# Optimization experiments

Measured on AMD Instinct MI355X. Metric: run time of the kernel, lower is better.

Reference implementation:

```python
import jax, jax.numpy as jnp
import numpy as np

B, S, D, H = 4, 1024, 1024, 16
HD = D // H  # head_dim = 64


def setup_inputs() -> dict:
    key = jax.random.key(0)
    ks = jax.random.split(key, 16)
    w = lambda k: jax.random.normal(k, (D, D), dtype=jnp.float32) * 0.02
    b = lambda k: jax.random.normal(k, (D,), dtype=jnp.float32) * 0.02
    x = jax.random.normal(ks[0], (B, S, D), dtype=jnp.float32)
    mask = jnp.tril(jnp.ones((S, S), dtype=jnp.int32))[None, None]  # causal [1,1,S,S]
    bar_indices = jax.random.randint(ks[1], (S,), 0, S, dtype=jnp.int64)
    beat_indices = jax.random.randint(ks[2], (S,), 0, S, dtype=jnp.int64)
    return {
        "x": x, "mask": mask, "bar_indices": bar_indices, "beat_indices": beat_indices,
        "Wq": w(ks[3]), "bq": b(ks[4]), "Wk": w(ks[5]), "bk": b(ks[6]),
        "Wv": w(ks[7]), "bv": b(ks[8]),
        "W_bark": w(ks[9]), "b_bark": b(ks[10]),
        "W_beatk": w(ks[11]), "b_beatk": b(ks[12]),
        "Wo": w(ks[13]), "bo": b(ks[14]),
    }


def reference(x, mask, bar_indices, beat_indices, Wq, bq, Wk, bk, Wv, bv,
              W_bark, b_bark, W_beatk, b_beatk, Wo, bo):
    Bs, Sl, Dm = x.shape
    heads, hd = H, Dm // H

    def proj(t, W, b):  # torch Linear: t @ W.T + b, then split heads -> [B,H,S,hd]
        y = t @ W.T + b
        return y.reshape(Bs, -1, heads, hd).transpose(0, 2, 1, 3)

    q = proj(x, Wq, bq)
    k = proj(x, Wk, bk)
    v = proj(x, Wv, bv)
    scale = 1.0 / jnp.sqrt(jnp.asarray(hd, x.dtype))

    scores = jnp.einsum('bhqd,bhkd->bhqk', q, k) * scale

    # hierarchical bar bias (bar_query is computed but unused in the original)
    bar_k = proj(x[:, bar_indices], W_bark, b_bark)
    scores = scores + 0.2 * (jnp.einsum('bhqd,bhkd->bhqk', q, bar_k) * scale)

    # hierarchical beat bias
    beat_k = proj(x[:, beat_indices], W_beatk, b_beatk)
    scores = scores + 0.1 * (jnp.einsum('bhqd,bhkd->bhqk', q, beat_k) * scale)

    scores = jnp.where(mask == 0, jnp.asarray(-1e9, scores.dtype), scores)
    attn = jax.nn.softmax(scores, axis=-1)  # dropout is identity in eval

    out = jnp.einsum('bhqk,bhkd->bhqd', attn, v)
    out = out.transpose(0, 2, 1, 3).reshape(Bs, Sl, Dm)
    return out @ Wo.T + bo
```

## Files before the change

kernel.cpp:

```cpp
#include <hip/hip_runtime.h>
#include <hip/hip_bf16.h>


typedef __bf16 bf16x8 __attribute__((ext_vector_type(8)));
typedef __bf16 bf16x4 __attribute__((ext_vector_type(4)));
typedef float  f32x4  __attribute__((ext_vector_type(4)));

#define DMODEL 1024

#define ASYNC_LOAD16(gp, lp)                                                  \
    __builtin_amdgcn_global_load_lds(                                         \
        (const __attribute__((address_space(1))) unsigned int*)(gp),          \
        (__attribute__((address_space(3))) unsigned int*)(lp), 16, 0, 0)

__global__ __launch_bounds__(256) void cvt_kernel(
    const float* __restrict__ x,
    const float* __restrict__ Wq, const float* __restrict__ Wk,
    const float* __restrict__ Wv, const float* __restrict__ Wbar,
    const float* __restrict__ Wbeat, const float* __restrict__ Wo,
    __bf16* __restrict__ dst)
{
    const int g = blockIdx.x * 256 + threadIdx.x;
    const size_t e = (size_t)g * 8;
    const int seg = (int)(e >> 20);
    const float* src; size_t off; float s = 1.0f;
    if (seg < 4)       { src = x;     off = e; }
    else if (seg == 4) { src = Wq;    off = e - ((size_t)4 << 20); }
    else if (seg == 5) { src = Wk;    off = e - ((size_t)5 << 20); }
    else if (seg == 6) { src = Wv;    off = e - ((size_t)6 << 20); }
    else if (seg == 7) { src = Wbar;  off = e - ((size_t)7 << 20); s = 0.2f; }
    else if (seg == 8) { src = Wbeat; off = e - ((size_t)8 << 20); s = 0.1f; }
    else               { src = Wo;    off = e - ((size_t)9 << 20); }
    const float4 a = *(const float4*)&src[off];
    const float4 b = *(const float4*)&src[off + 4];
    bf16x8 v;
    v[0] = (__bf16)(a.x * s); v[1] = (__bf16)(a.y * s);
    v[2] = (__bf16)(a.z * s); v[3] = (__bf16)(a.w * s);
    v[4] = (__bf16)(b.x * s); v[5] = (__bf16)(b.y * s);
    v[6] = (__bf16)(b.z * s); v[7] = (__bf16)(b.w * s);
    *(bf16x8*)&dst[e] = v;
}


#define SWZ_COL(r_, ks_) \
    (((((ks_) * 64) + quad * 16) ^ (((r_) & 7) << 4)) >> 1)

#define READ_A(c_, mh_)                                                       \
    do {                                                                      \
        _Pragma("unroll") for (int mi = 0; mi < 2; ++mi) {                    \
            const int r_ = ((w >> 2) << 5) + (mh_) * 64 + mi * 16 + l15;      \
            _Pragma("unroll") for (int ks = 0; ks < 2; ++ks)                  \
                af[mi][ks] = *(const bf16x8*)&Alds[(c_) * 8192 + r_ * 64 +    \
                                                   SWZ_COL(r_, ks)];          \
        }                                                                     \
    } while (0)

#define READ_B(c_, nh_)                                                       \
    do {                                                                      \
        _Pragma("unroll") for (int nj = 0; nj < 2; ++nj) {                    \
            const int r_ = ((w & 3) << 5) + (nh_) * 128 + nj * 16 + l15;      \
            _Pragma("unroll") for (int ks = 0; ks < 2; ++ks)                  \
                bf[nj][ks] = *(const bf16x8*)&Blds[(c_) * 16384 + r_ * 64 +   \
                                                    SWZ_COL(r_, ks)];         \
        }                                                                     \
    } while (0)

#define STAGE_A8(bufn_, h_, kt_)                                              \
    do {                                                                      \
        const int tm_ = (kt_) >> 4;                                           \
        const int k0_ = ((kt_) & 15) << 6;                                    \
        const __bf16* ap_ = (tm_ == 0) ? aA0##h_ : (tm_ == 1) ? aA1##h_       \
                                                              : aA2##h_;      \
        ASYNC_LOAD16(ap_ + k0_,                                               \
                     &Alds[(bufn_) * 8192 + (h_) * 4096 + w * 512]);          \
    } while (0)

#define STAGE_B8(bufn_, h_, kt_)                                              \
    do {                                                                      \
        const int tm_ = (kt_) >> 4;                                           \
        const int k0_ = ((kt_) & 15) << 6;                                    \
        const __bf16* wp_ = (tm_ == 0) ? W0 : (tm_ == 1) ? W1 : W2;           \
        ASYNC_LOAD16(wp_ + bro##h_##0 + k0_,                                  \
                     &Blds[(bufn_) * 16384 + (h_) * 8192 + w * 512]);         \
        ASYNC_LOAD16(wp_ + bro##h_##1 + k0_,                                  \
                     &Blds[(bufn_) * 16384 + (h_) * 8192 + 4096 + w * 512]);  \
    } while (0)

#define PHASE_BAR1()                                                          \
    do {                                                                      \
        __builtin_amdgcn_s_barrier();                                         \
        asm volatile("s_waitcnt lgkmcnt(0)" ::: "memory");                    \
    } while (0)

#define MFMA8(mh_, nh_)                                                       \
    do {                                                                      \
        __builtin_amdgcn_s_setprio(1);                                        \
        _Pragma("unroll") for (int mi = 0; mi < 2; ++mi)                      \
        _Pragma("unroll") for (int nj = 0; nj < 2; ++nj) {                    \
            acc[(mh_)*2 + mi][(nh_)*2 + nj] =                                 \
                __builtin_amdgcn_mfma_f32_16x16x32_bf16(                      \
                    af[mi][0], bf[nj][0], acc[(mh_)*2 + mi][(nh_)*2 + nj],    \
                    0, 0, 0);                                                 \
            acc[(mh_)*2 + mi][(nh_)*2 + nj] =                                 \
                __builtin_amdgcn_mfma_f32_16x16x32_bf16(                      \
                    af[mi][1], bf[nj][1], acc[(mh_)*2 + mi][(nh_)*2 + nj],    \
                    0, 0, 0);                                                 \
        }                                                                     \
        __builtin_amdgcn_s_setprio(0);                                        \
    } while (0)

__global__ __launch_bounds__(512, 2) void gemm8p_kernel(
    const __bf16* __restrict__ xb,
    const __bf16* __restrict__ Wqb, const __bf16* __restrict__ Wkb,
    const __bf16* __restrict__ Wvb, const __bf16* __restrict__ Wbarb,
    const __bf16* __restrict__ Wbeatb,
    const float* __restrict__ bq, const float* __restrict__ bk,
    const float* __restrict__ bv, const float* __restrict__ bbar,
    const float* __restrict__ bbeat,
    const int* __restrict__ bar_idx, const int* __restrict__ beat_idx,
    __bf16* __restrict__ qbuf, __bf16* __restrict__ keffbuf,
    __bf16* __restrict__ vtbuf)
{
    __shared__ __align__(16) __bf16 Alds[2 * 8192];
    __shared__ __align__(16) __bf16 Blds[2 * 16384];

    const int bid = blockIdx.x;
    int mode, tk;
    if (bid < 128)      { mode = 1; tk = bid; }
    else if (bid < 256) { mode = 0; tk = bid - 128; }
    else                { mode = 2; tk = bid - 256; }
    const int m0 = (tk >> 2) << 7;
    const int n0 = (tk & 3) << 8;
    const int nkt = (mode == 1) ? 48 : 16;

    const int t    = (int)threadIdx.x;
    const int w    = t >> 6;
    const int lane = t & 63;
    const int l15  = lane & 15;
    const int quad = lane >> 4;

    const int srow = t >> 3;
    const int scol = ((((t & 7) * 16) ^ (((t >> 3) & 7) << 4)) >> 1);

    const __bf16* aA00 = xb + (size_t)(m0 + srow) * DMODEL + scol;
    const __bf16* aA01 = xb + (size_t)(m0 + 64 + srow) * DMODEL + scol;
    const __bf16* aA10 = aA00; const __bf16* aA11 = aA01;
    const __bf16* aA20 = aA00; const __bf16* aA21 = aA01;
    const __bf16 *W0, *W1, *W2;
    if (mode == 0)      { W0 = W1 = W2 = Wqb; }
    else if (mode == 2) { W0 = W1 = W2 = Wvb; }
    else {
        W0 = Wkb; W1 = Wbarb; W2 = Wbeatb;
        const int bb = m0 & ~1023;
        const int lr = m0 & 1023;
        aA10 = xb + (size_t)(bb + bar_idx[lr + srow]) * DMODEL + scol;
        aA11 = xb + (size_t)(bb + bar_idx[lr + 64 + srow]) * DMODEL + scol;
        aA20 = xb + (size_t)(bb + beat_idx[lr + srow]) * DMODEL + scol;
        aA21 = xb + (size_t)(bb + beat_idx[lr + 64 + srow]) * DMODEL + scol;
    }
    const size_t bro00 = (size_t)(n0 + srow) * DMODEL + scol;
    const size_t bro01 = (size_t)(n0 + 64 + srow) * DMODEL + scol;
    const size_t bro10 = (size_t)(n0 + 128 + srow) * DMODEL + scol;
    const size_t bro11 = (size_t)(n0 + 192 + srow) * DMODEL + scol;

    f32x4 acc[4][4];
#pragma unroll
    for (int i = 0; i < 4; ++i)
#pragma unroll
        for (int j = 0; j < 4; ++j)
            acc[i][j] = {0.f, 0.f, 0.f, 0.f};
    bf16x8 af[2][2], bf[2][2];

    STAGE_A8(0, 0, 0);
    asm volatile("" ::: "memory");
    STAGE_B8(0, 0, 0);
    asm volatile("" ::: "memory");
    STAGE_B8(0, 1, 0);
    asm volatile("" ::: "memory");
    STAGE_A8(0, 1, 0);
    asm volatile("s_waitcnt vmcnt(3)" ::: "memory");
    __builtin_amdgcn_s_barrier();

#pragma unroll 1
    for (int kt = 0; kt < nkt - 1; ++kt) {
        const int c  = kt & 1;
        const int nb = c ^ 1;
        const int kn = kt + 1;

        READ_A(c, 0);
        READ_B(c, 0);
        STAGE_A8(nb, 0, kn);
        PHASE_BAR1();
        MFMA8(0, 0);
        asm volatile("s_waitcnt vmcnt(2)" ::: "memory");
        __builtin_amdgcn_s_barrier();

        READ_B(c, 1);
        STAGE_B8(nb, 0, kn);
        PHASE_BAR1();
        MFMA8(0, 1);
        asm volatile("s_waitcnt vmcnt(3)" ::: "memory");
        __builtin_amdgcn_s_barrier();

        READ_A(c, 1);
        STAGE_B8(nb, 1, kn);
        PHASE_BAR1();
        MFMA8(1, 1);
        __builtin_amdgcn_s_barrier();

        READ_B(c, 0);
        STAGE_A8(nb, 1, kn);
        PHASE_BAR1();
        MFMA8(1, 0);
        asm volatile("s_waitcnt vmcnt(3)" ::: "memory");
        __builtin_amdgcn_s_barrier();
    }

    {
        const int c = (nkt - 1) & 1;
        READ_A(c, 0);
        READ_B(c, 0);
        PHASE_BAR1();
        MFMA8(0, 0);
        asm volatile("s_waitcnt vmcnt(1)" ::: "memory");
        __builtin_amdgcn_s_barrier();

        READ_B(c, 1);
        PHASE_BAR1();
        MFMA8(0, 1);
        asm volatile("s_waitcnt vmcnt(0)" ::: "memory");
        __builtin_amdgcn_s_barrier();

        READ_A(c, 1);
        PHASE_BAR1();
        MFMA8(1, 1);
        __builtin_amdgcn_s_barrier();

        READ_B(c, 0);
        PHASE_BAR1();
        MFMA8(1, 0);
    }

#pragma unroll
    for (int an = 0; an < 4; ++an) {
        const int col = n0 + ((w & 3) << 5) + (an >> 1) * 128 +
                        (an & 1) * 16 + l15;
        float bias;
        if (mode == 0)      bias = bq[col];
        else if (mode == 1) bias = bk[col] + 0.2f * bbar[col] + 0.1f * bbeat[col];
        else                bias = bv[col];
#pragma unroll
        for (int am = 0; am < 4; ++am) {
            const int rowbase = m0 + ((w >> 2) << 5) + (am >> 1) * 64 +
                                (am & 1) * 16 + quad * 4;
            if (mode == 2) {
                const int bb = rowbase >> 10;
                const int sb = rowbase & 1023;
                bf16x4 vv;
#pragma unroll
                for (int r = 0; r < 4; ++r) vv[r] = (__bf16)(acc[am][an][r] + bias);
                *(bf16x4*)&vtbuf[((size_t)(bb * 1024 + col)) * 1024 + sb] = vv;
            } else if (mode == 0) {
#pragma unroll
                for (int r = 0; r < 4; ++r)
                    qbuf[(size_t)(rowbase + r) * DMODEL + col] =
                        (__bf16)((acc[am][an][r] + bias) * 0.125f);
            } else {
#pragma unroll
                for (int r = 0; r < 4; ++r)
                    keffbuf[(size_t)(rowbase + r) * DMODEL + col] =
                        (__bf16)(acc[am][an][r] + bias);
            }
        }
    }
}

__global__ __launch_bounds__(256) void oproj_kernel(
    const __bf16* __restrict__ attnb, const __bf16* __restrict__ Wob,
    const float* __restrict__ bo, float* __restrict__ outb)
{
    const int tile = blockIdx.x;
    const int m0 = (tile >> 3) << 6;
    const int n0 = (tile & 7) << 7;

    __shared__ __align__(16) __bf16 Alds[64 * 32];
    __shared__ __align__(16) __bf16 Blds[128 * 32];

    const int t    = threadIdx.x;
    const int w    = t >> 6;
    const int lane = t & 63;
    const int l15  = lane & 15;
    const int quad = lane >> 4;
    const int wm   = (w >> 1) << 5;
    const int wn   = (w & 1) << 6;
    const int srow = t >> 2;
    const int scol = ((((t & 3) * 16) ^ (((t >> 2) & 3) << 4)) >> 1);
    const int rcol = (((quad * 16) ^ ((l15 & 3) << 4)) >> 1);

    const __bf16* gA  = attnb + (size_t)(m0 + srow) * DMODEL + scol;
    const __bf16* gB0 = Wob + (size_t)(n0 + srow) * DMODEL + scol;
    const __bf16* gB1 = Wob + (size_t)(n0 + 64 + srow) * DMODEL + scol;
    __bf16* lA  = &Alds[w * 512];
    __bf16* lB0 = &Blds[w * 512];
    __bf16* lB1 = &Blds[2048 + w * 512];

    f32x4 acc[2][4];
    for (int i = 0; i < 2; ++i)
        for (int j = 0; j < 4; ++j)
            acc[i][j] = {0.f, 0.f, 0.f, 0.f};

    for (int kk = 0; kk < 32; ++kk) {
        const int k0 = kk * 32;
        ASYNC_LOAD16(gA + k0, lA);
        ASYNC_LOAD16(gB0 + k0, lB0);
        ASYNC_LOAD16(gB1 + k0, lB1);
        __syncthreads();

        bf16x8 af[2], bfr[4];
        for (int i = 0; i < 2; ++i)
            af[i] = *(const bf16x8*)&Alds[(wm + i * 16 + l15) * 32 + rcol];
        for (int j = 0; j < 4; ++j)
            bfr[j] = *(const bf16x8*)&Blds[(wn + j * 16 + l15) * 32 + rcol];

        for (int i = 0; i < 2; ++i)
            for (int j = 0; j < 4; ++j)
                acc[i][j] = __builtin_amdgcn_mfma_f32_16x16x32_bf16(
                    af[i], bfr[j], acc[i][j], 0, 0, 0);
        __syncthreads();
    }

    for (int j = 0; j < 4; ++j) {
        const int col = n0 + wn + j * 16 + l15;
        const float bias = bo[col];
        for (int i = 0; i < 2; ++i) {
            const int rowbase = m0 + wm + i * 16 + quad * 4;
            for (int r = 0; r < 4; ++r)
                outb[(size_t)(rowbase + r) * DMODEL + col] = acc[i][j][r] + bias;
        }
    }
}

__global__ __launch_bounds__(256) void attn_kernel(
    const __bf16* __restrict__ qbuf, const __bf16* __restrict__ keffbuf,
    const __bf16* __restrict__ vtbuf, __bf16* __restrict__ attnbuf)
{
    const int bh = blockIdx.y;
    const int b  = bh >> 4;
    const int h  = bh & 15;
    const int qt = blockIdx.x;
    const int q0 = qt * 64;

    __shared__ __align__(16) __bf16 Klds[64][72];
    __shared__ __align__(16) __bf16 Vlds[64][72];
    __shared__ __align__(16) __bf16 Plds[4][16][72];

    const int t    = threadIdx.x;
    const int w    = t >> 6;
    const int lane = t & 63;
    const int l15  = lane & 15;
    const int quad = lane >> 4;

    const __bf16* qbase =
        qbuf + (size_t)(b * 1024 + q0 + w * 16 + l15) * DMODEL + h * 64;
    bf16x8 qf0 = *(const bf16x8*)&qbase[quad * 8];
    bf16x8 qf1 = *(const bf16x8*)&qbase[32 + quad * 8];

    bf16x8 ones;
    for (int i = 0; i < 8; ++i) ones[i] = (__bf16)1.0f;

    f32x4 o[4];
    for (int i = 0; i < 4; ++i) o[i] = {0.f, 0.f, 0.f, 0.f};
    f32x4 lacc = {0.f, 0.f, 0.f, 0.f};

    const int srow = t >> 2;
    const int scol = (t & 3) * 16;

    const __bf16* kbase = keffbuf + (size_t)(b * 1024) * DMODEL + h * 64;
    const __bf16* vtb   = vtbuf + (size_t)(b * 1024 + h * 64) * 1024;

    for (int j = 0; j <= qt; ++j) {
        const __bf16* kg = kbase + (size_t)(j * 64 + srow) * DMODEL + scol;
        *(bf16x8*)&Klds[srow][scol]     = *(const bf16x8*)kg;
        *(bf16x8*)&Klds[srow][scol + 8] = *(const bf16x8*)(kg + 8);
        const __bf16* vg = vtb + (size_t)srow * 1024 + j * 64 + scol;
        *(bf16x8*)&Vlds[srow][scol]     = *(const bf16x8*)vg;
        *(bf16x8*)&Vlds[srow][scol + 8] = *(const bf16x8*)(vg + 8);
        __syncthreads();

        f32x4 sc[4];
        for (int nt = 0; nt < 4; ++nt) {
            sc[nt] = {0.f, 0.f, 0.f, 0.f};
            bf16x8 kf0 = *(const bf16x8*)&Klds[nt * 16 + l15][quad * 8];
            bf16x8 kf1 = *(const bf16x8*)&Klds[nt * 16 + l15][32 + quad * 8];
            sc[nt] = __builtin_amdgcn_mfma_f32_16x16x32_bf16(qf0, kf0, sc[nt], 0, 0, 0);
            sc[nt] = __builtin_amdgcn_mfma_f32_16x16x32_bf16(qf1, kf1, sc[nt], 0, 0, 0);
        }

        if (j == qt) {
            const int qrow_base = q0 + w * 16 + quad * 4;
            for (int nt = 0; nt < 4; ++nt) {
                const int kcol = j * 64 + nt * 16 + l15;
                for (int r = 0; r < 4; ++r)
                    if (kcol > qrow_base + r) sc[nt][r] = -1e30f;
            }
        }

        for (int nt = 0; nt < 4; ++nt)
            for (int r = 0; r < 4; ++r)
                sc[nt][r] = __expf(sc[nt][r]);

        for (int nt = 0; nt < 4; ++nt)
            for (int r = 0; r < 4; ++r)
                Plds[w][quad * 4 + r][nt * 16 + l15] = (__bf16)sc[nt][r];
        asm volatile("s_waitcnt lgkmcnt(0)" ::: "memory");

        bf16x8 pf0 = *(const bf16x8*)&Plds[w][l15][quad * 8];
        bf16x8 pf1 = *(const bf16x8*)&Plds[w][l15][32 + quad * 8];

        lacc = __builtin_amdgcn_mfma_f32_16x16x32_bf16(pf0, ones, lacc, 0, 0, 0);
        lacc = __builtin_amdgcn_mfma_f32_16x16x32_bf16(pf1, ones, lacc, 0, 0, 0);

        for (int nd = 0; nd < 4; ++nd) {
            bf16x8 vf0 = *(const bf16x8*)&Vlds[nd * 16 + l15][quad * 8];
            bf16x8 vf1 = *(const bf16x8*)&Vlds[nd * 16 + l15][32 + quad * 8];
            o[nd] = __builtin_amdgcn_mfma_f32_16x16x32_bf16(pf0, vf0, o[nd], 0, 0, 0);
            o[nd] = __builtin_amdgcn_mfma_f32_16x16x32_bf16(pf1, vf1, o[nd], 0, 0, 0);
        }
        __syncthreads();
    }

    float rinv[4];
    for (int r = 0; r < 4; ++r) rinv[r] = 1.0f / lacc[r];
    for (int nd = 0; nd < 4; ++nd) {
        for (int r = 0; r < 4; ++r) {
            const int row = q0 + w * 16 + quad * 4 + r;
            attnbuf[(size_t)(b * 1024 + row) * DMODEL + h * 64 + nd * 16 + l15] =
                (__bf16)(o[nd][r] * rinv[r]);
        }
    }
}

extern "C" void kernel_launch(void* const* d_in, const int* in_sizes, int n_in,
                              void* d_out, int out_size, void* d_ws, size_t ws_size,
                              hipStream_t stream) {
    const float* x     = (const float*)d_in[0];
    const int* bar     = (const int*)d_in[2];
    const int* beat    = (const int*)d_in[3];
    const float* Wq    = (const float*)d_in[4];
    const float* bq    = (const float*)d_in[5];
    const float* Wk    = (const float*)d_in[6];
    const float* bk    = (const float*)d_in[7];
    const float* Wv    = (const float*)d_in[8];
    const float* bv    = (const float*)d_in[9];
    const float* Wbar  = (const float*)d_in[10];
    const float* bbar  = (const float*)d_in[11];
    const float* Wbeat = (const float*)d_in[12];
    const float* bbeat = (const float*)d_in[13];
    const float* Wo    = (const float*)d_in[14];
    const float* bo    = (const float*)d_in[15];

    const size_t M1 = (size_t)1 << 20;
    __bf16* xb     = (__bf16*)d_ws;
    __bf16* Wqb    = xb + 4 * M1;
    __bf16* Wkb    = Wqb + M1;
    __bf16* Wvb    = Wkb + M1;
    __bf16* Wbarb  = Wvb + M1;
    __bf16* Wbeatb = Wbarb + M1;
    __bf16* Wob    = Wbeatb + M1;
    __bf16* qbuf   = Wob + M1;
    __bf16* keff   = qbuf + 4 * M1;
    __bf16* vt     = keff + 4 * M1;
    __bf16* attn   = vt + 4 * M1;
    float*  outb   = (float*)d_out;

    cvt_kernel<<<5120, 256, 0, stream>>>(x, Wq, Wk, Wv, Wbar, Wbeat, Wo, xb);

    gemm8p_kernel<<<384, 512, 0, stream>>>(
        xb, Wqb, Wkb, Wvb, Wbarb, Wbeatb,
        bq, bk, bv, bbar, bbeat, bar, beat,
        qbuf, keff, vt);

    attn_kernel<<<dim3(16, 64), 256, 0, stream>>>(qbuf, keff, vt, attn);

    oproj_kernel<<<512, 256, 0, stream>>>(attn, Wob, bo, outb);
}
```

Before: 241.8 us.

## Triple-buffer projection GEMM LDS and read full fragments once per k-tile

Replaces the double-buffered, four-phase projection GEMM main loop with a triple-buffered loop that prefetches two k-tiles ahead. Each k-tile now loads all A and B fragments from LDS up front and issues the MFMAs in two halves, with two barriers per tile instead of four. The goal is to hide global-load latency better and spend less time in barriers. In exchange, LDS use grows from 96 KB to 144 KB per block, which probably breaks the two-blocks-per-CU occupancy, and more fragment registers are live at once.

After: 221.5 us. -8.4%, faster.

```diff
diff --git a/kernel.cpp b/kernel.cpp
--- a/kernel.cpp
+++ b/kernel.cpp
@@ -45,27 +45,25 @@
 #define SWZ_COL(r_, ks_) \
     (((((ks_) * 64) + quad * 16) ^ (((r_) & 7) << 4)) >> 1)
 
-#define READ_A(c_, mh_)                                                       \
+#define READ_ALL(c_)                                                          \
     do {                                                                      \
+        _Pragma("unroll") for (int mh = 0; mh < 2; ++mh)                      \
         _Pragma("unroll") for (int mi = 0; mi < 2; ++mi) {                    \
-            const int r_ = ((w >> 2) << 5) + (mh_) * 64 + mi * 16 + l15;      \
+            const int r_ = ((w >> 2) << 5) + mh * 64 + mi * 16 + l15;         \
             _Pragma("unroll") for (int ks = 0; ks < 2; ++ks)                  \
-                af[mi][ks] = *(const bf16x8*)&Alds[(c_) * 8192 + r_ * 64 +    \
-                                                   SWZ_COL(r_, ks)];          \
+                af[mh][mi][ks] = *(const bf16x8*)&Alds[(c_) * 8192 +          \
+                                        r_ * 64 + SWZ_COL(r_, ks)];           \
+        }                                                                     \
+        _Pragma("unroll") for (int nh = 0; nh < 2; ++nh)                      \
+        _Pragma("unroll") for (int nj = 0; nj < 2; ++nj) {                    \
+            const int r_ = ((w & 3) << 5) + nh * 128 + nj * 16 + l15;         \
+            _Pragma("unroll") for (int ks = 0; ks < 2; ++ks)                  \
+                bfr[nh][nj][ks] = *(const bf16x8*)&Blds[(c_) * 16384 +        \
+                                        r_ * 64 + SWZ_COL(r_, ks)];           \
         }                                                                     \
     } while (0)
 
-#define READ_B(c_, nh_)                                                       \
-    do {                                                                      \
-        _Pragma("unroll") for (int nj = 0; nj < 2; ++nj) {                    \
-            const int r_ = ((w & 3) << 5) + (nh_) * 128 + nj * 16 + l15;      \
-            _Pragma("unroll") for (int ks = 0; ks < 2; ++ks)                  \
-                bf[nj][ks] = *(const bf16x8*)&Blds[(c_) * 16384 + r_ * 64 +   \
-                                                    SWZ_COL(r_, ks)];         \
-        }                                                                     \
-    } while (0)
-
-#define STAGE_A8(bufn_, h_, kt_)                                              \
+#define STAGE_A1(bufn_, h_, kt_)                                              \
     do {                                                                      \
         const int tm_ = (kt_) >> 4;                                           \
         const int k0_ = ((kt_) & 15) << 6;                                    \
@@ -75,7 +73,7 @@
                      &Alds[(bufn_) * 8192 + (h_) * 4096 + w * 512]);          \
     } while (0)
 
-#define STAGE_B8(bufn_, h_, kt_)                                              \
+#define STAGE_B2(bufn_, h_, kt_)                                              \
     do {                                                                      \
         const int tm_ = (kt_) >> 4;                                           \
         const int k0_ = ((kt_) & 15) << 6;                                    \
@@ -92,19 +90,17 @@
         asm volatile("s_waitcnt lgkmcnt(0)" ::: "memory");                    \
     } while (0)
 
-#define MFMA8(mh_, nh_)                                                       \
+#define MFMA16(nh_)                                                           \
     do {                                                                      \
         __builtin_amdgcn_s_setprio(1);                                        \
+        _Pragma("unroll") for (int mh = 0; mh < 2; ++mh)                      \
         _Pragma("unroll") for (int mi = 0; mi < 2; ++mi)                      \
-        _Pragma("unroll") for (int nj = 0; nj < 2; ++nj) {                    \
-            acc[(mh_)*2 + mi][(nh_)*2 + nj] =                                 \
+        _Pragma("unroll") for (int nj = 0; nj < 2; ++nj)                      \
+        _Pragma("unroll") for (int ks = 0; ks < 2; ++ks) {                    \
+            acc[mh * 2 + mi][(nh_) * 2 + nj] =                                \
                 __builtin_amdgcn_mfma_f32_16x16x32_bf16(                      \
-                    af[mi][0], bf[nj][0], acc[(mh_)*2 + mi][(nh_)*2 + nj],    \
-                    0, 0, 0);                                                 \
-            acc[(mh_)*2 + mi][(nh_)*2 + nj] =                                 \
-                __builtin_amdgcn_mfma_f32_16x16x32_bf16(                      \
-                    af[mi][1], bf[nj][1], acc[(mh_)*2 + mi][(nh_)*2 + nj],    \
-                    0, 0, 0);                                                 \
+                    af[mh][mi][ks], bfr[(nh_)][nj][ks],                       \
+                    acc[mh * 2 + mi][(nh_) * 2 + nj], 0, 0, 0);               \
         }                                                                     \
         __builtin_amdgcn_s_setprio(0);                                        \
     } while (0)
@@ -121,8 +117,8 @@
     __bf16* __restrict__ qbuf, __bf16* __restrict__ keffbuf,
     __bf16* __restrict__ vtbuf)
 {
-    __shared__ __align__(16) __bf16 Alds[2 * 8192];
-    __shared__ __align__(16) __bf16 Blds[2 * 16384];
+    __shared__ __align__(16) __bf16 Alds[3 * 8192];
+    __shared__ __align__(16) __bf16 Blds[3 * 16384];
 
     const int bid = blockIdx.x;
     int mode, tk;
@@ -169,76 +165,41 @@
 #pragma unroll
         for (int j = 0; j < 4; ++j)
             acc[i][j] = {0.f, 0.f, 0.f, 0.f};
-    bf16x8 af[2][2], bf[2][2];
-
-    STAGE_A8(0, 0, 0);
+    bf16x8 af[2][2][2], bfr[2][2][2];
+
+    STAGE_A1(0, 0, 0);
+    STAGE_A1(0, 1, 0);
+    STAGE_B2(0, 0, 0);
+    STAGE_B2(0, 1, 0);
     asm volatile("" ::: "memory");
-    STAGE_B8(0, 0, 0);
-    asm volatile("" ::: "memory");
-    STAGE_B8(0, 1, 0);
-    asm volatile("" ::: "memory");
-    STAGE_A8(0, 1, 0);
-    asm volatile("s_waitcnt vmcnt(3)" ::: "memory");
+    STAGE_A1(1, 0, 1);
+    STAGE_A1(1, 1, 1);
+    STAGE_B2(1, 0, 1);
+    STAGE_B2(1, 1, 1);
+    asm volatile("s_waitcnt vmcnt(6)" ::: "memory");
     __builtin_amdgcn_s_barrier();
 
+    int rc = 0, fc = 2;
 #pragma unroll 1
-    for (int kt = 0; kt < nkt - 1; ++kt) {
-        const int c  = kt & 1;
-        const int nb = c ^ 1;
-        const int kn = kt + 1;
-
-        READ_A(c, 0);
-        READ_B(c, 0);
-        STAGE_A8(nb, 0, kn);
+    for (int kt = 0; kt < nkt; ++kt) {
+        const int kn = kt + 2;
+        const bool st = (kn < nkt);
+
+        READ_ALL(rc);
+        if (st) { STAGE_A1(fc, 0, kn); STAGE_A1(fc, 1, kn); }
         PHASE_BAR1();
-        MFMA8(0, 0);
-        asm volatile("s_waitcnt vmcnt(2)" ::: "memory");
-        __builtin_amdgcn_s_barrier();
-
-        READ_B(c, 1);
-        STAGE_B8(nb, 0, kn);
+        MFMA16(0);
+
+        if (st) { STAGE_B2(fc, 0, kn); STAGE_B2(fc, 1, kn); }
+        if (kt < nkt - 2)
+            asm volatile("s_waitcnt vmcnt(6)" ::: "memory");
+        else if (kt == nkt - 2)
+            asm volatile("s_waitcnt vmcnt(0)" ::: "memory");
         PHASE_BAR1();
-        MFMA8(0, 1);
-        asm volatile("s_waitcnt vmcnt(3)" ::: "memory");
-        __builtin_amdgcn_s_barrier();
-
-        READ_A(c, 1);
-        STAGE_B8(nb, 1, kn);
-        PHASE_BAR1();
-        MFMA8(1, 1);
-        __builtin_amdgcn_s_barrier();
-
-        READ_B(c, 0);
-        STAGE_A8(nb, 1, kn);
-        PHASE_BAR1();
-        MFMA8(1, 0);
-        asm volatile("s_waitcnt vmcnt(3)" ::: "memory");
-        __builtin_amdgcn_s_barrier();
-    }
-
-    {
-        const int c = (nkt - 1) & 1;
-        READ_A(c, 0);
-        READ_B(c, 0);
-        PHASE_BAR1();
-        MFMA8(0, 0);
-        asm volatile("s_waitcnt vmcnt(1)" ::: "memory");
-        __builtin_amdgcn_s_barrier();
-
-        READ_B(c, 1);
-        PHASE_BAR1();
-        MFMA8(0, 1);
-        asm volatile("s_waitcnt vmcnt(0)" ::: "memory");
-        __builtin_amdgcn_s_barrier();
-
-        READ_A(c, 1);
-        PHASE_BAR1();
-        MFMA8(1, 1);
-        __builtin_amdgcn_s_barrier();
-
-        READ_B(c, 0);
-        PHASE_BAR1();
-        MFMA8(1, 0);
+        MFMA16(1);
+
+        rc = (rc == 2) ? 0 : rc + 1;
+        fc = (fc == 2) ? 0 : fc + 1;
     }
 
 #pragma unroll
```
